# Optimization experiments

Measured on AMD Instinct MI355X. Metric: run time of the kernel, lower is better.

## Reference

```python
import math
import jax, jax.numpy as jnp
import numpy as np

EPS = 1e-9


def _abeles(q, thickness, roughness, sld):
    # q: (B,Q) float32; thickness, roughness: (B,L) float32; sld: (B,L+1) float32
    sld_c = sld.astype(jnp.complex64)
    amb = sld_c[:, 0:1]
    sld_comp = (sld_c - amb) * 1e-6 + 1j * 1e-9          # (B, L+1)
    q_in = q[..., None].astype(jnp.complex64)             # (B, Q, 1)
    sld_in = sld_comp[:, None, :]                         # (B, 1, L+1)
    t_in = thickness[:, None, :]                          # (B, 1, L)
    r_in = roughness[:, None, :]                          # (B, 1, L)

    k_n = jnp.sqrt((q_in / 2.0) ** 2 - 4.0 * math.pi * sld_in)  # (B, Q, L+1)
    k_curr, k_next = k_n[..., :-1], k_n[..., 1:]                # (B, Q, L)

    beta = 1j * t_in * k_curr
    exp_beta = jnp.exp(beta)
    exp_m_beta = jnp.exp(-beta)
    r_n = (k_curr - k_next) / (k_curr + k_next + EPS) * jnp.exp(-2.0 * k_curr * k_next * r_in ** 2)

    m00 = exp_beta          # (B, Q, L)
    m01 = r_n * exp_beta
    m10 = r_n * exp_m_beta
    m11 = exp_m_beta

    # sequential 2x2 complex matrix product over the layer axis (Parratt/Abeles recursion)
    init = (m00[..., 0], m01[..., 0], m10[..., 0], m11[..., 0])
    ms = tuple(jnp.moveaxis(m[..., 1:], -1, 0) for m in (m00, m01, m10, m11))  # each (L-1, B, Q)

    def step(carry, m):
        a, b, c, d = carry
        e, f, g, h = m
        return (a * e + b * g, a * f + b * h, c * e + d * g, c * f + d * h), None

    (a00, a01, a10, a11), _ = jax.lax.scan(step, init, ms)
    quot = a10 / (a00 + EPS)
    return quot.real ** 2 + quot.imag ** 2                # (B, Q) float32


def setup_inputs() -> dict:
    key = jax.random.key(0)
    k1, k2, k3, k4 = jax.random.split(key, 4)
    B, Q, L = 128, 2048, 64
    q = jax.random.uniform(k1, (B, Q), dtype=jnp.float32) * 0.3 + 0.005   # q-range ~ XRR
    thickness = jax.random.uniform(k2, (B, L), dtype=jnp.float32) * 100.0 + 10.0
    roughness = jax.random.uniform(k3, (B, L), dtype=jnp.float32) * 5.0
    sld = jax.random.normal(k4, (B, L + 1), dtype=jnp.float32) * 2.0
    return {"q": q, "thickness": thickness, "roughness": roughness, "sld": sld}


def reference(q, thickness, roughness, sld):
    return _abeles(q, thickness, roughness, sld)
```

## Files before the change

kernel.cpp:

```cpp
#include <hip/hip_runtime.h>
#include <math.h>

typedef float v2f __attribute__((ext_vector_type(2)));

#define EPSF 1e-9f
#define FOUR_PI 12.566370614359172f
#define YIM (-(FOUR_PI * 1e-9f))
#define LOG2E  1.4426950408889634f
#define INV2PI 0.15915494309189535f

__device__ __forceinline__ float frcp(float x) { return __builtin_amdgcn_rcpf(x); }
__device__ __forceinline__ float frsq(float x) { return __builtin_amdgcn_rsqf(x); }
__device__ __forceinline__ float fsq(float x)  { return __builtin_amdgcn_sqrtf(x); }

#if __has_builtin(__builtin_amdgcn_exp2f)
__device__ __forceinline__ float fexp2(float x) { return __builtin_amdgcn_exp2f(x); }
#else
__device__ __forceinline__ float fexp2(float x) { return exp2f(x); }
#endif
#if __has_builtin(__builtin_amdgcn_sinf) && __has_builtin(__builtin_amdgcn_cosf)
__device__ __forceinline__ float fsin_rev(float x) { return __builtin_amdgcn_sinf(x); }
__device__ __forceinline__ float fcos_rev(float x) { return __builtin_amdgcn_cosf(x); }
#else
__device__ __forceinline__ float fsin_rev(float x) { return __sinf(x * 6.283185307179586f); }
__device__ __forceinline__ float fcos_rev(float x) { return __cosf(x * 6.283185307179586f); }
#endif
#if __has_builtin(__builtin_amdgcn_fractf)
__device__ __forceinline__ float ffract(float x) { return __builtin_amdgcn_fractf(x); }
#else
__device__ __forceinline__ float ffract(float x) { return x - floorf(x); }
#endif

__device__ __forceinline__ v2f vfma(v2f a, v2f b, v2f c) { return __builtin_elementwise_fma(a, b, c); }
__device__ __forceinline__ v2f vabs(v2f a) { return __builtin_elementwise_abs(a); }

__device__ __forceinline__ void csqrt2(v2f x, v2f& u, v2f& v) {
    v2f r;
    r.x = fsq(fmaf(x.x, x.x, YIM * YIM));
    r.y = fsq(fmaf(x.y, x.y, YIM * YIM));
    v2f h = 0.5f * (r + vabs(x));
    v2f irs; irs.x = frsq(h.x); irs.y = frsq(h.y);
    v2f w = h * irs;
    v2f o = (0.5f * YIM) * irs;
    u.x = (x.x >= 0.0f) ? w.x : -o.x;
    v.x = (x.x >= 0.0f) ? o.x : -w.x;
    u.y = (x.y >= 0.0f) ? w.y : -o.y;
    v.y = (x.y >= 0.0f) ? o.y : -w.y;
}

#define RENORM() do {                                            \
    v2f m_ = vabs(Dr) + vabs(Di);                                \
    int ex_ = (__float_as_int(m_.x) >> 23) & 0xff;               \
    int ey_ = (__float_as_int(m_.y) >> 23) & 0xff;               \
    v2f s_;                                                      \
    s_.x = __int_as_float((254 - ex_) << 23);                    \
    s_.y = __int_as_float((254 - ey_) << 23);                    \
    Nr *= s_; Ni *= s_; Dr *= s_; Di *= s_;                      \
} while (0)

__global__ __launch_bounds__(256, 2) void abeles_kernel(
    const float* __restrict__ qarr,
    const float* __restrict__ thick,
    const float* __restrict__ rough,
    const float* __restrict__ sld,
    float* __restrict__ out,
    int Q, int L)
{
    const int b  = blockIdx.y;
    const int tx = threadIdx.x;

    __shared__ float  s_xp[65];
    __shared__ float4 s_pk[64];

    {
        float s0 = sld[(size_t)b * (L + 1)];
        for (int i = tx; i < L + 1; i += blockDim.x)
            s_xp[i] = (FOUR_PI * 1e-6f) * (sld[(size_t)b * (L + 1) + i] - s0);
        for (int i = tx; i < L; i += blockDim.x) {
            float t  = thick[(size_t)b * L + i];
            float sg = rough[(size_t)b * L + i];
            float s2 = sg * sg;
            s_pk[i] = make_float4(2.0f * t * LOG2E, 2.0f * t * INV2PI,
                                  -2.0f * s2 * LOG2E, -2.0f * s2);
        }
    }

    const int iq0 = blockIdx.x * (2 * blockDim.x) + tx;
    const int iq1 = iq0 + blockDim.x;
    float qa = (iq0 < Q) ? qarr[(size_t)b * Q + iq0] : 0.1f;
    float qb = (iq1 < Q) ? qarr[(size_t)b * Q + iq1] : 0.1f;
    v2f q2; q2.x = 0.25f * qa * qa; q2.y = 0.25f * qb * qb;
    __syncthreads();

    v2f cu, cv;
    csqrt2(q2 - s_xp[L], cu, cv);
    v2f Nr = (v2f)0.0f, Ni = (v2f)0.0f, Dr = (v2f)1.0f, Di = (v2f)0.0f;

    int j = L;
    while (j >= 8) {
        const int g = j - 8;

        v2f ku[8], kv[8];
        #pragma unroll
        for (int t = 0; t < 8; ++t)
            csqrt2(q2 - s_xp[g + t], ku[t], kv[t]);

        v2f Ar[8], Ai[8], Er[8], Ei[8], Pr[8], Pi[8];
        #pragma unroll
        for (int t = 7; t >= 0; --t) {
            v2f u1 = ku[t], v1 = kv[t];
            v2f u2 = (t == 7) ? cu : ku[t + 1];
            v2f v2_ = (t == 7) ? cv : kv[t + 1];
            const float4 P = s_pk[g + t];

            v2f nr = u1 - u2, ni = v1 - v2_;
            Er[t] = u1 + u2 + EPSF; Ei[t] = v1 + v2_;

            v2f kkr = vfma(u1, u2, -(v1 * v2_));
            v2f kki = vfma(u1, v2_, v1 * u2);
            v2f ew; ew.x = fexp2(P.z * kkr.x); ew.y = fexp2(P.z * kkr.y);
            v2f a  = P.w * kki;
            v2f a2 = a * a;
            v2f cw = vfma(a2, (v2f)(-0.5f), (v2f)1.0f);
            v2f sw = a * vfma(a2, (v2f)(-0.16666667f), (v2f)1.0f);
            v2f fr = ew * cw, fi = ew * sw;
            Ar[t] = vfma(nr, fr, -(ni * fi));
            Ai[t] = vfma(nr, fi, ni * fr);

            v2f pm; pm.x = fexp2(P.x * v1.x); pm.y = fexp2(P.x * v1.y);
            v2f cp, sp;
            {
                float pax = ffract(P.y * u1.x), pay = ffract(P.y * u1.y);
                cp.x = fcos_rev(pax); sp.x = fsin_rev(pax);
                cp.y = fcos_rev(pay); sp.y = fsin_rev(pay);
            }
            Pr[t] = pm * cp;
            Pi[t] = -pm * sp;
        }

        #pragma unroll
        for (int t = 7; t >= 0; --t) {
            v2f tnr = vfma(Ar[t], Dr, vfma(-Ai[t], Di, vfma(Er[t], Nr, -(Ei[t] * Ni))));
            v2f tni = vfma(Ar[t], Di, vfma( Ai[t], Dr, vfma(Er[t], Ni,   Ei[t] * Nr)));
            v2f tdr = vfma(Er[t], Dr, vfma(-Ei[t], Di, vfma(Ar[t], Nr, -(Ai[t] * Ni))));
            v2f tdi = vfma(Er[t], Di, vfma( Ei[t], Dr, vfma(Ar[t], Ni,   Ai[t] * Nr)));
            Nr = vfma(tnr, Pr[t], -(tni * Pi[t]));
            Ni = vfma(tnr, Pi[t],   tni * Pr[t]);
            Dr = tdr; Di = tdi;
            if (t == 4 || t == 0) RENORM();
        }

        cu = ku[0]; cv = kv[0];
        j = g;
    }

    while (j > 0) {
        --j;
        v2f u1, v1;
        csqrt2(q2 - s_xp[j], u1, v1);
        const float4 P = s_pk[j];
        v2f nr = u1 - cu, ni = v1 - cv;
        v2f er = u1 + cu + EPSF, ei = v1 + cv;
        v2f kkr = vfma(u1, cu, -(v1 * cv));
        v2f kki = vfma(u1, cv, v1 * cu);
        v2f ew; ew.x = fexp2(P.z * kkr.x); ew.y = fexp2(P.z * kkr.y);
        v2f a = P.w * kki, a2 = a * a;
        v2f cw = vfma(a2, (v2f)(-0.5f), (v2f)1.0f);
        v2f sw = a * vfma(a2, (v2f)(-0.16666667f), (v2f)1.0f);
        v2f fr = ew * cw, fi = ew * sw;
        v2f Arv = vfma(nr, fr, -(ni * fi));
        v2f Aiv = vfma(nr, fi, ni * fr);
        v2f pm; pm.x = fexp2(P.x * v1.x); pm.y = fexp2(P.x * v1.y);
        float pax = ffract(P.y * u1.x), pay = ffract(P.y * u1.y);
        v2f cp, sp;
        cp.x = fcos_rev(pax); sp.x = fsin_rev(pax);
        cp.y = fcos_rev(pay); sp.y = fsin_rev(pay);
        v2f pr = pm * cp, pi = -pm * sp;
        v2f tnr = vfma(Arv, Dr, vfma(-Aiv, Di, vfma(er, Nr, -(ei * Ni))));
        v2f tni = vfma(Arv, Di, vfma( Aiv, Dr, vfma(er, Ni,   ei * Nr)));
        v2f tdr = vfma(er, Dr, vfma(-ei, Di, vfma(Arv, Nr, -(Aiv * Ni))));
        v2f tdi = vfma(er, Di, vfma( ei, Dr, vfma(Arv, Ni,   Aiv * Nr)));
        Nr = vfma(tnr, pr, -(tni * pi));
        Ni = vfma(tnr, pi,   tni * pr);
        Dr = tdr; Di = tdi;
        RENORM();
        cu = u1; cv = v1;
    }

    v2f d2 = vfma(Dr, Dr, Di * Di);
    v2f n2 = vfma(Nr, Nr, Ni * Ni);
    if (iq0 < Q) out[(size_t)b * Q + iq0] = n2.x * frcp(d2.x);
    if (iq1 < Q) out[(size_t)b * Q + iq1] = n2.y * frcp(d2.y);
}

extern "C" void kernel_launch(void* const* d_in, const int* in_sizes, int n_in,
                              void* d_out, int out_size, void* d_ws, size_t ws_size,
                              hipStream_t stream) {
    const float* q     = (const float*)d_in[0];
    const float* thick = (const float*)d_in[1];
    const float* rough = (const float*)d_in[2];
    const float* sld   = (const float*)d_in[3];
    float* out = (float*)d_out;

    int B = in_sizes[3] - in_sizes[1];
    int L = in_sizes[1] / B;
    int Q = in_sizes[0] / B;

    dim3 block(256);
    dim3 grid((Q + 511) / 512, B);
    abeles_kernel<<<grid, block, 0, stream>>>(q, thick, rough, sld, out, Q, L);
}
```

Measured before the change: 28.40 us.

## Software-pipeline layer groups: build next group's factors while sweeping current

Replaces the 8-layer batch loop with 4-layer groups that are double-buffered: the per-layer transfer factors for the next group (complex sqrt, exp, sin/cos) are computed while the sequential matrix sweep of the current group runs. This lets transcendental work interleave with the dependent FMA chain and exposes more instruction-level parallelism. It also drops the EPS added to the k sum, which removes an add but could risk a division-like degeneracy. It adds register pressure from holding two groups of factors, which may hurt occupancy under the 256x2 launch bound.

Measured after the change: 34.46 us. 21.3% more time.

```diff
diff --git a/kernel.cpp b/kernel.cpp
--- a/kernel.cpp
+++ b/kernel.cpp
@@ -3,7 +3,6 @@
 
 typedef float v2f __attribute__((ext_vector_type(2)));
 
-#define EPSF 1e-9f
 #define FOUR_PI 12.566370614359172f
 #define YIM (-(FOUR_PI * 1e-9f))
 #define LOG2E  1.4426950408889634f
@@ -48,15 +47,69 @@
     v.y = (x.y >= 0.0f) ? o.y : -w.y;
 }
 
-#define RENORM() do {                                            \
-    v2f m_ = vabs(Dr) + vabs(Di);                                \
-    int ex_ = (__float_as_int(m_.x) >> 23) & 0xff;               \
-    int ey_ = (__float_as_int(m_.y) >> 23) & 0xff;               \
-    v2f s_;                                                      \
-    s_.x = __int_as_float((254 - ex_) << 23);                    \
-    s_.y = __int_as_float((254 - ey_) << 23);                    \
-    Nr *= s_; Ni *= s_; Dr *= s_; Di *= s_;                      \
-} while (0)
+struct IngG {
+    v2f Ar[4], Ai[4], Er[4], Ei[4], Pr[4], Pi[4];
+    v2f ku0, kv0;
+};
+
+__device__ __forceinline__ void make_ing(const float* __restrict__ s_xp,
+                                         const float4* __restrict__ s_pk,
+                                         int g, v2f q2, v2f cu, v2f cv, IngG& o)
+{
+    v2f ku[4], kv[4];
+    #pragma unroll
+    for (int t = 0; t < 4; ++t)
+        csqrt2(q2 - s_xp[g + t], ku[t], kv[t]);
+
+    #pragma unroll
+    for (int t = 3; t >= 0; --t) {
+        v2f u1 = ku[t], v1 = kv[t];
+        v2f u2 = (t == 3) ? cu : ku[t + 1];
+        v2f w2 = (t == 3) ? cv : kv[t + 1];
+        const float4 P = s_pk[g + t];
+
+        v2f nr = u1 - u2, ni = v1 - w2;
+        o.Er[t] = u1 + u2; o.Ei[t] = v1 + w2;
+
+        v2f kkr = vfma(u1, u2, -(v1 * w2));
+        v2f kki = vfma(u1, w2, v1 * u2);
+        v2f ew; ew.x = fexp2(P.z * kkr.x); ew.y = fexp2(P.z * kkr.y);
+        v2f a = P.w * kki, a2 = a * a;
+        v2f cw = vfma(a2, (v2f)(-0.5f), (v2f)1.0f);
+        v2f sw = a * vfma(a2, (v2f)(-0.16666667f), (v2f)1.0f);
+        v2f fr = ew * cw, fi = ew * sw;
+        o.Ar[t] = vfma(nr, fr, -(ni * fi));
+        o.Ai[t] = vfma(nr, fi, ni * fr);
+
+        v2f pm; pm.x = fexp2(P.x * v1.x); pm.y = fexp2(P.x * v1.y);
+        float pax = ffract(P.y * u1.x), pay = ffract(P.y * u1.y);
+        v2f cp, sp;
+        cp.x = fcos_rev(pax); cp.y = fcos_rev(pay);
+        sp.x = fsin_rev(pax); sp.y = fsin_rev(pay);
+        o.Pr[t] = pm * cp; o.Pi[t] = -pm * sp;
+    }
+    o.ku0 = ku[0]; o.kv0 = kv[0];
+}
+
+__device__ __forceinline__ void sweep(const IngG& I, v2f& Nr, v2f& Ni, v2f& Dr, v2f& Di)
+{
+    #pragma unroll
+    for (int t = 3; t >= 0; --t) {
+        v2f tnr = vfma(I.Ar[t], Dr, vfma(-I.Ai[t], Di, vfma(I.Er[t], Nr, -(I.Ei[t] * Ni))));
+        v2f tni = vfma(I.Ar[t], Di, vfma( I.Ai[t], Dr, vfma(I.Er[t], Ni,   I.Ei[t] * Nr)));
+        v2f tdr = vfma(I.Er[t], Dr, vfma(-I.Ei[t], Di, vfma(I.Ar[t], Nr, -(I.Ai[t] * Ni))));
+        v2f tdi = vfma(I.Er[t], Di, vfma( I.Ei[t], Dr, vfma(I.Ar[t], Ni,   I.Ai[t] * Nr)));
+        Nr = vfma(tnr, I.Pr[t], -(tni * I.Pi[t]));
+        Ni = vfma(tnr, I.Pi[t],   tni * I.Pr[t]);
+        Dr = tdr; Di = tdi;
+    }
+    v2f m = vabs(Dr) + vabs(Di);
+    int ex = (__float_as_int(m.x) >> 23) & 0xff;
+    int ey = (__float_as_int(m.y) >> 23) & 0xff;
+    v2f s; s.x = __int_as_float((254 - ex) << 23);
+    s.y = __int_as_float((254 - ey) << 23);
+    Nr *= s; Ni *= s; Dr *= s; Di *= s;
+}
 
 __global__ __launch_bounds__(256, 2) void abeles_kernel(
     const float* __restrict__ qarr,
@@ -97,61 +150,21 @@
     v2f Nr = (v2f)0.0f, Ni = (v2f)0.0f, Dr = (v2f)1.0f, Di = (v2f)0.0f;
 
     int j = L;
-    while (j >= 8) {
-        const int g = j - 8;
-
-        v2f ku[8], kv[8];
-        #pragma unroll
-        for (int t = 0; t < 8; ++t)
-            csqrt2(q2 - s_xp[g + t], ku[t], kv[t]);
-
-        v2f Ar[8], Ai[8], Er[8], Ei[8], Pr[8], Pi[8];
-        #pragma unroll
-        for (int t = 7; t >= 0; --t) {
-            v2f u1 = ku[t], v1 = kv[t];
-            v2f u2 = (t == 7) ? cu : ku[t + 1];
-            v2f v2_ = (t == 7) ? cv : kv[t + 1];
-            const float4 P = s_pk[g + t];
-
-            v2f nr = u1 - u2, ni = v1 - v2_;
-            Er[t] = u1 + u2 + EPSF; Ei[t] = v1 + v2_;
-
-            v2f kkr = vfma(u1, u2, -(v1 * v2_));
-            v2f kki = vfma(u1, v2_, v1 * u2);
-            v2f ew; ew.x = fexp2(P.z * kkr.x); ew.y = fexp2(P.z * kkr.y);
-            v2f a  = P.w * kki;
-            v2f a2 = a * a;
-            v2f cw = vfma(a2, (v2f)(-0.5f), (v2f)1.0f);
-            v2f sw = a * vfma(a2, (v2f)(-0.16666667f), (v2f)1.0f);
-            v2f fr = ew * cw, fi = ew * sw;
-            Ar[t] = vfma(nr, fr, -(ni * fi));
-            Ai[t] = vfma(nr, fi, ni * fr);
-
-            v2f pm; pm.x = fexp2(P.x * v1.x); pm.y = fexp2(P.x * v1.y);
-            v2f cp, sp;
-            {
-                float pax = ffract(P.y * u1.x), pay = ffract(P.y * u1.y);
-                cp.x = fcos_rev(pax); sp.x = fsin_rev(pax);
-                cp.y = fcos_rev(pay); sp.y = fsin_rev(pay);
-            }
-            Pr[t] = pm * cp;
-            Pi[t] = -pm * sp;
+    if (j >= 8) {
+        IngG A, B;
+        make_ing(s_xp, s_pk, j - 4, q2, cu, cv, A);
+        j -= 4;
+        bool aLive = true;
+        while (j >= 4) {
+            if (aLive) { make_ing(s_xp, s_pk, j - 4, q2, A.ku0, A.kv0, B);
+                         sweep(A, Nr, Ni, Dr, Di); }
+            else       { make_ing(s_xp, s_pk, j - 4, q2, B.ku0, B.kv0, A);
+                         sweep(B, Nr, Ni, Dr, Di); }
+            aLive = !aLive;
+            j -= 4;
         }
-
-        #pragma unroll
-        for (int t = 7; t >= 0; --t) {
-            v2f tnr = vfma(Ar[t], Dr, vfma(-Ai[t], Di, vfma(Er[t], Nr, -(Ei[t] * Ni))));
-            v2f tni = vfma(Ar[t], Di, vfma( Ai[t], Dr, vfma(Er[t], Ni,   Ei[t] * Nr)));
-            v2f tdr = vfma(Er[t], Dr, vfma(-Ei[t], Di, vfma(Ar[t], Nr, -(Ai[t] * Ni))));
-            v2f tdi = vfma(Er[t], Di, vfma( Ei[t], Dr, vfma(Ar[t], Ni,   Ai[t] * Nr)));
-            Nr = vfma(tnr, Pr[t], -(tni * Pi[t]));
-            Ni = vfma(tnr, Pi[t],   tni * Pr[t]);
-            Dr = tdr; Di = tdi;
-            if (t == 4 || t == 0) RENORM();
-        }
-
-        cu = ku[0]; cv = kv[0];
-        j = g;
+        if (aLive) { sweep(A, Nr, Ni, Dr, Di); cu = A.ku0; cv = A.kv0; }
+        else       { sweep(B, Nr, Ni, Dr, Di); cu = B.ku0; cv = B.kv0; }
     }
 
     while (j > 0) {
@@ -160,7 +173,7 @@
         csqrt2(q2 - s_xp[j], u1, v1);
         const float4 P = s_pk[j];
         v2f nr = u1 - cu, ni = v1 - cv;
-        v2f er = u1 + cu + EPSF, ei = v1 + cv;
+        v2f er = u1 + cu, ei = v1 + cv;
         v2f kkr = vfma(u1, cu, -(v1 * cv));
         v2f kki = vfma(u1, cv, v1 * cu);
         v2f ew; ew.x = fexp2(P.z * kkr.x); ew.y = fexp2(P.z * kkr.y);
@@ -183,7 +196,14 @@
         Nr = vfma(tnr, pr, -(tni * pi));
         Ni = vfma(tnr, pi,   tni * pr);
         Dr = tdr; Di = tdi;
-        RENORM();
+        {
+            v2f m = vabs(Dr) + vabs(Di);
+            int ex = (__float_as_int(m.x) >> 23) & 0xff;
+            int ey = (__float_as_int(m.y) >> 23) & 0xff;
+            v2f s; s.x = __int_as_float((254 - ex) << 23);
+            s.y = __int_as_float((254 - ey) << 23);
+            Nr *= s; Ni *= s; Dr *= s; Di *= s;
+        }
         cu = u1; cv = v1;
     }
 
```
